# Kernel optimization log

Measured on AMD Instinct MI355X. Metric: run time of the kernel, lower is better.

## Reference

```python
import jax, jax.numpy as jnp
import numpy as np

N_MIN = 16
N_TABLES = 16
PER_LEVEL_SCALE = 1.3195079565048218
MAX_TABLE = 2 ** 19
H1, H2, H3 = 1, 2654435761, 805459861
OFFS = np.array([[0,0,0],[0,0,1],[0,1,0],[0,1,1],[1,0,0],[1,0,1],[1,1,0],[1,1,1]], dtype=np.int32)

def _levels():
    N_l, sizes, max_direct = [], [], 0
    for i in range(N_TABLES):
        res = int(np.ceil(N_MIN * np.exp(i * np.log(PER_LEVEL_SCALE)) - 1.0)) + 1
        ts = res ** 3
        ts = ts if ts % 8 == 0 else ((ts + 7) // 8) * 8
        ts = min(MAX_TABLE, ts)
        if ts == res ** 3:
            max_direct = i
        N_l.append(res); sizes.append(ts)
    return N_l, sizes, max_direct

N_L, SIZES, MAX_DIRECT = _levels()

def hash_encode(pos, grids):
    # pos: [N,3] in [0,1); grids: [16, MAX_TABLE, 2] (levels padded to MAX_TABLE)
    feats = []
    for l in range(N_TABLES):
        uvz = pos * jnp.float32(N_L[l])
        iuv_f = jnp.floor(uvz)
        f = uvz - iuv_f                                   # fractional part [N,3]
        corners = iuv_f.astype(jnp.int32)[:, None, :] + OFFS[None]  # [N,8,3]
        if l <= MAX_DIRECT:
            R = N_L[l]
            idx = (corners[..., 2] * (R * R) + corners[..., 1] * R + corners[..., 0]) % SIZES[l]
        else:
            cu = corners.astype(jnp.uint32)
            h = (cu[..., 0] * jnp.uint32(H1)) ^ (cu[..., 1] * jnp.uint32(H2)) ^ (cu[..., 2] * jnp.uint32(H3))
            idx = (h % jnp.uint32(SIZES[l])).astype(jnp.int32)
        c = grids[l][idx]                                 # gather -> [N,8,2]
        fx, fy, fz = f[:, 0:1], f[:, 1:2], f[:, 2:3]
        c00 = c[:, 0] * (1 - fx) + c[:, 4] * fx
        c01 = c[:, 1] * (1 - fx) + c[:, 5] * fx
        c10 = c[:, 2] * (1 - fx) + c[:, 6] * fx
        c11 = c[:, 3] * (1 - fx) + c[:, 7] * fx
        c0 = c00 * (1 - fy) + c10 * fy
        c1 = c01 * (1 - fy) + c11 * fy
        feats.append(c0 * (1 - fz) + c1 * fy)  # NOTE: c1*fy (not fz) replicates source exactly
    return jnp.concatenate(feats, axis=-1)  # [N, 32]

def setup_inputs():
    key = jax.random.key(0)
    ks = jax.random.split(key, 7)
    N = 1048576  # max_samples(512) * batch_size(2048)
    x = jax.random.uniform(ks[0], (N, 19), dtype=jnp.float32)  # pos(3) in [0,1) + dir feats(16)
    grids = (jax.random.uniform(ks[1], (N_TABLES, MAX_TABLE, 2), dtype=jnp.float32) * 2.0 - 1.0) * 1e-4
    h = 64
    w_sigma1 = jax.random.normal(ks[2], (32, h), dtype=jnp.float32) / np.sqrt(32).astype(np.float32)
    w_sigma2 = jax.random.normal(ks[3], (h, 16), dtype=jnp.float32) / np.sqrt(h).astype(np.float32)
    w_c1 = jax.random.normal(ks[4], (32, h), dtype=jnp.float32) / np.sqrt(32).astype(np.float32)
    w_c2 = jax.random.normal(ks[5], (h, h), dtype=jnp.float32) / np.sqrt(h).astype(np.float32)
    w_c3 = jax.random.normal(ks[6], (h, 3), dtype=jnp.float32) / np.sqrt(h).astype(np.float32)
    return {"x": x, "grids": grids, "w_sigma1": w_sigma1, "w_sigma2": w_sigma2,
            "w_c1": w_c1, "w_c2": w_c2, "w_c3": w_c3}

def reference(x, grids, w_sigma1, w_sigma2, w_c1, w_c2, w_c3):
    pos, direc = x[:, :3], x[:, 3:]
    enc = hash_encode(pos, grids)                       # [N,32]
    out = jax.nn.relu(enc @ w_sigma1) @ w_sigma2        # [N,16]
    sigma = out[:, 0]
    ci = jnp.concatenate([direc, out], axis=-1)         # [N,32]
    color = jax.nn.sigmoid(jax.nn.relu(jax.nn.relu(ci @ w_c1) @ w_c2) @ w_c3)  # [N,3]
    return jnp.concatenate([color, sigma[:, None]], axis=-1)  # [N,4]
```

## Files before the change

kernel.cpp:

```cpp
#include <hip/hip_runtime.h>
#include <math.h>


#define BLOCK 256
#define NTAB  (16*524288)
#define PITCH 88

constexpr int      kNL[16] = {16,22,28,37,49,65,85,112,148,195,257,338,446,589,777,1025};
constexpr unsigned kSZ[16] = {4096u,10648u,21952u,50656u,117656u,274632u,
                              524288u,524288u,524288u,524288u,524288u,
                              524288u,524288u,524288u,524288u,524288u};

typedef __attribute__((ext_vector_type(8))) short short8;
typedef __attribute__((ext_vector_type(4))) float float4v;

__device__ __forceinline__ short f2bf(float f) {
    unsigned u = __float_as_uint(f);
    unsigned r = u + 0x7fffu + ((u >> 16) & 1u);
    return (short)(r >> 16);
}
__device__ __forceinline__ float bf2f(short h) {
    return __uint_as_float(((unsigned)(unsigned short)h) << 16);
}
__device__ __forceinline__ unsigned pk2(float a, float b) {
    return ((unsigned)(unsigned short)f2bf(b) << 16) | (unsigned)(unsigned short)f2bf(a);
}
__device__ __forceinline__ float pe0(unsigned u) { return __uint_as_float(u << 16); }
__device__ __forceinline__ float pe1(unsigned u) { return __uint_as_float(u & 0xffff0000u); }

__global__ void pack_pos(const float* __restrict__ x, float4* __restrict__ pos4, int n)
{
    int i = blockIdx.x * BLOCK + threadIdx.x;
    if (i >= n) return;
    const float* xr = x + (size_t)i * 19;
    pos4[i] = make_float4(xr[0], xr[1], xr[2], 0.f);
}

__global__ void conv_tables(const float* __restrict__ grids, unsigned* __restrict__ tbu)
{
    int i = blockIdx.x * BLOCK + threadIdx.x;
    if (i >= NTAB) return;
    float2 v = ((const float2*)grids)[i];
    tbu[i] = pk2(v.x, v.y);
}

__global__ void pack_wfrag(const float* __restrict__ w1, const float* __restrict__ w2,
                           const float* __restrict__ wc1, const float* __restrict__ wc2,
                           const float* __restrict__ wc3, uint4* __restrict__ wf)
{
    int lane = threadIdx.x;
    if (lane >= 64) return;
    int cn = lane & 15, q = lane >> 4;

    auto pack8 = [](const float* src, int stride) -> uint4 {
        uint4 r;
        r.x = pk2(src[0*stride], src[1*stride]);
        r.y = pk2(src[2*stride], src[3*stride]);
        r.z = pk2(src[4*stride], src[5*stride]);
        r.w = pk2(src[6*stride], src[7*stride]);
        return r;
    };

    int f = 0;
    for (int nt = 0; nt < 4; ++nt)
        wf[(f++)*64 + lane] = pack8(w1 + (q*8)*64 + nt*16 + cn, 64);
    for (int c = 0; c < 2; ++c)
        wf[(f++)*64 + lane] = pack8(w2 + (c*32 + q*8)*16 + cn, 16);
    for (int nt = 0; nt < 4; ++nt)
        wf[(f++)*64 + lane] = pack8(wc1 + (q*8)*64 + nt*16 + cn, 64);
    for (int c = 0; c < 2; ++c)
        for (int nt = 0; nt < 4; ++nt)
            wf[(f++)*64 + lane] = pack8(wc2 + (c*32 + q*8)*64 + nt*16 + cn, 64);
    for (int c = 0; c < 2; ++c) {
        if (cn < 3) wf[(f++)*64 + lane] = pack8(wc3 + (c*32 + q*8)*3 + cn, 3);
        else { uint4 z; z.x = z.y = z.z = z.w = 0u; wf[(f++)*64 + lane] = z; }
    }
}

template<int L>
__device__ __forceinline__ void gather4(const float4* __restrict__ pos4,
                                        const unsigned* __restrict__ tball,
                                        unsigned* __restrict__ encu,
                                        int n, int p0, int cnt)
{
    constexpr int R = kNL[L];
    constexpr unsigned S = kSZ[L];
    constexpr unsigned H2c = 2654435761u, H3c = 805459861u;
    const unsigned* __restrict__ tbu = tball + (size_t)L * 524288u;

    unsigned vv[4][8];
    float fxa[4], fya[4], fza[4];
    #pragma unroll
    for (int q = 0; q < 4; ++q) {
        if (q >= cnt) continue;
        float4 p = pos4[p0+q];
        const float Rf = (float)R;
        float ux = p.x*Rf, uy = p.y*Rf, uz = p.z*Rf;
        float gx = floorf(ux), gy = floorf(uy), gz = floorf(uz);
        fxa[q] = ux-gx; fya[q] = uy-gy; fza[q] = uz-gz;
        int ix = (int)gx, iy = (int)gy, iz = (int)gz;

        if (L >= 6) {
            unsigned tc[4];
            #pragma unroll
            for (int c = 0; c < 4; ++c) {
                int yb = c >> 1, zb = c & 1;
                tc[c] = (unsigned)(iy+yb)*H2c ^ (unsigned)(iz+zb)*H3c;
            }
            if ((ix & 1) == 0) {
                #pragma unroll
                for (int c = 0; c < 4; ++c) {
                    unsigned idx0 = ((unsigned)ix ^ tc[c]) & (S-1u);
                    uint2 pr = *(const uint2*)(tbu + (idx0 & ~1u));
                    unsigned swp = idx0 & 1u;
                    vv[q][c]   = swp ? pr.y : pr.x;
                    vv[q][4+c] = swp ? pr.x : pr.y;
                }
            } else {
                #pragma unroll
                for (int c = 0; c < 4; ++c) {
                    unsigned idx0 = ((unsigned)ix     ^ tc[c]) & (S-1u);
                    unsigned idx1 = ((unsigned)(ix+1) ^ tc[c]) & (S-1u);
                    vv[q][c]   = tbu[idx0];
                    vv[q][4+c] = tbu[idx1];
                }
            }
        } else if (L >= 3) {
            #pragma unroll
            for (int j = 0; j < 8; ++j) {
                int ox = ix + ((j>>2)&1);
                int oy = iy + ((j>>1)&1);
                int oz = iz + (j&1);
                unsigned h = (unsigned)ox ^ (unsigned)oy*H2c ^ (unsigned)oz*H3c;
                vv[q][j] = tbu[h % S];
            }
        } else {
            #pragma unroll
            for (int j = 0; j < 8; ++j) {
                int ox = ix + ((j>>2)&1);
                int oy = iy + ((j>>1)&1);
                int oz = iz + (j&1);
                vv[q][j] = tbu[(unsigned)((oz*(R*R) + oy*R + ox) % (int)S)];
            }
        }
    }

    unsigned pkd[4];
    #pragma unroll
    for (int q = 0; q < 4; ++q) {
        if (q >= cnt) continue;
        const float fx = fxa[q], fy = fya[q], fz = fza[q];
        const float w0x = 1.f-fx, w0y = 1.f-fy, w0z = 1.f-fz;
        float e0, e1;
        {
            float c00 = pe0(vv[q][0])*w0x + pe0(vv[q][4])*fx;
            float c01 = pe0(vv[q][1])*w0x + pe0(vv[q][5])*fx;
            float c10 = pe0(vv[q][2])*w0x + pe0(vv[q][6])*fx;
            float c11 = pe0(vv[q][3])*w0x + pe0(vv[q][7])*fx;
            float c0 = c00*w0y + c10*fy;
            float c1 = c01*w0y + c11*fy;
            e0 = c0*w0z + c1*fy;
        }
        {
            float c00 = pe1(vv[q][0])*w0x + pe1(vv[q][4])*fx;
            float c01 = pe1(vv[q][1])*w0x + pe1(vv[q][5])*fx;
            float c10 = pe1(vv[q][2])*w0x + pe1(vv[q][6])*fx;
            float c11 = pe1(vv[q][3])*w0x + pe1(vv[q][7])*fx;
            float c0 = c00*w0y + c10*fy;
            float c1 = c01*w0y + c11*fy;
            e1 = c0*w0z + c1*fy;
        }
        pkd[q] = pk2(e0, e1);
    }

    unsigned* d = encu + (size_t)L*n + p0;
    if (cnt == 4) {
        uint4 o; o.x = pkd[0]; o.y = pkd[1]; o.z = pkd[2]; o.w = pkd[3];
        *(uint4*)d = o;
    } else {
        for (int q = 0; q < cnt; ++q) d[q] = pkd[q];
    }
}

__global__ __launch_bounds__(BLOCK)
void enc_all(const float4* __restrict__ pos4, const unsigned* __restrict__ tball,
             unsigned* __restrict__ encu, int n, int byA, int byB)
{
    const int bx = blockIdx.x;
    const int by = blockIdx.y;

    if (by < byA) {
        int p0 = (by*BLOCK + threadIdx.x) * 4;
        if (p0 >= n) return;
        int cnt = min(4, n - p0);
        switch (bx) {
            case 0: gather4< 6>(pos4,tball,encu,n,p0,cnt); break;
            case 1: gather4< 7>(pos4,tball,encu,n,p0,cnt); break;
            case 2: gather4< 8>(pos4,tball,encu,n,p0,cnt); break;
            case 3: gather4< 9>(pos4,tball,encu,n,p0,cnt); break;
            case 4: gather4<10>(pos4,tball,encu,n,p0,cnt); break;
            case 5: gather4<11>(pos4,tball,encu,n,p0,cnt); break;
            case 6: gather4<12>(pos4,tball,encu,n,p0,cnt); break;
            case 7: gather4<13>(pos4,tball,encu,n,p0,cnt); break;
        }
    } else if (by < byA + byB) {
        int q4 = (n + 3) / 4;
        int quarter = bx & 3;
        int jb = quarter * q4;
        int je = min(n, jb + q4);
        int p0 = jb + ((by-byA)*BLOCK + threadIdx.x) * 4;
        if (p0 >= je) return;
        int cnt = min(4, je - p0);
        if (bx < 4) gather4<14>(pos4,tball,encu,n,p0,cnt);
        else        gather4<15>(pos4,tball,encu,n,p0,cnt);
    } else {
        int cj = (by - byA - byB)*8 + bx;
        if (cj >= 6*byA) return;
        int level = cj % 6;
        int chunk = cj / 6;
        int p0 = (chunk*BLOCK + threadIdx.x) * 4;
        if (p0 >= n) return;
        int cnt = min(4, n - p0);
        switch (level) {
            case 0: gather4<0>(pos4,tball,encu,n,p0,cnt); break;
            case 1: gather4<1>(pos4,tball,encu,n,p0,cnt); break;
            case 2: gather4<2>(pos4,tball,encu,n,p0,cnt); break;
            case 3: gather4<3>(pos4,tball,encu,n,p0,cnt); break;
            case 4: gather4<4>(pos4,tball,encu,n,p0,cnt); break;
            case 5: gather4<5>(pos4,tball,encu,n,p0,cnt); break;
        }
    }
}

__device__ __forceinline__ short8 ldfrag(const uint4* __restrict__ wf, int f, int lane) {
    union { uint4 u; short8 s; } cv;
    cv.u = wf[f*64 + lane];
    return cv.s;
}

__global__ __launch_bounds__(BLOCK)
void mlp_mfma(const float* __restrict__ x,
              const unsigned* __restrict__ encu,
              const uint4* __restrict__ wf,
              float* __restrict__ out, int n)
{
    __shared__ unsigned short s_scr[4][2][16*PITCH];
    __shared__ float s_sig[4][16];
    __shared__ float s_col[4][16][4];

    const int t = threadIdx.x;
    const int lane = t & 63;
    const int wave = t >> 6;
    const int m = lane & 15;
    const int q = lane >> 4;
    const int cn = m;
    const int blk = blockIdx.x * 64;
    const int pt  = blk + wave*16 + m;
    const int ptc = pt < n ? pt : n - 1;

    const float4v zero = {0.f, 0.f, 0.f, 0.f};

    union { unsigned u[4]; short8 s; } a1;
    #pragma unroll
    for (int i = 0; i < 4; ++i)
        a1.u[i] = encu[(size_t)(q*4 + i)*n + ptc];

    short8 bw1[4], bw2[2], bwc1[4];
    #pragma unroll
    for (int nt = 0; nt < 4; ++nt) bw1[nt] = ldfrag(wf, nt, lane);
    #pragma unroll
    for (int c = 0; c < 2; ++c)    bw2[c]  = ldfrag(wf, 4 + c, lane);
    #pragma unroll
    for (int nt = 0; nt < 4; ++nt) bwc1[nt] = ldfrag(wf, 6 + nt, lane);

    float4v h[4];
    #pragma unroll
    for (int nt = 0; nt < 4; ++nt) {
        h[nt] = __builtin_amdgcn_mfma_f32_16x16x32_bf16(a1.s, bw1[nt], zero, 0, 0, 0);
        #pragma unroll
        for (int r = 0; r < 4; ++r) h[nt][r] = fmaxf(h[nt][r], 0.f);
    }

    unsigned short* sA = &s_scr[wave][0][0];
    unsigned short* sB = &s_scr[wave][1][0];
    #pragma unroll
    for (int nt = 0; nt < 4; ++nt)
        #pragma unroll
        for (int r = 0; r < 4; ++r)
            sA[(q*4+r)*PITCH + nt*16 + cn] = (unsigned short)f2bf(h[nt][r]);
    short8 ah[2];
    #pragma unroll
    for (int c = 0; c < 2; ++c)
        ah[c] = *(const short8*)&sA[m*PITCH + c*32 + q*8];

    float4v o = __builtin_amdgcn_mfma_f32_16x16x32_bf16(ah[0], bw2[0], zero, 0, 0, 0);
    o = __builtin_amdgcn_mfma_f32_16x16x32_bf16(ah[1], bw2[1], o, 0, 0, 0);
    if (cn == 0) {
        #pragma unroll
        for (int r = 0; r < 4; ++r) s_sig[wave][q*4+r] = o[r];
    }

    #pragma unroll
    for (int r = 0; r < 4; ++r)
        sB[(q*4+r)*PITCH + cn] = (unsigned short)f2bf(o[r]);
    short8 ov = *(const short8*)&sB[m*PITCH + (q >= 2 ? (q-2)*8 : 0)];

    union { unsigned u[4]; short8 s; } ci_hi, ci_lo;
    if (q < 2) {
        #pragma unroll
        for (int i = 0; i < 4; ++i) {
            float d0 = x[(size_t)ptc*19 + 3 + q*8 + 2*i];
            float d1 = x[(size_t)ptc*19 + 3 + q*8 + 2*i + 1];
            short h0 = f2bf(d0), h1 = f2bf(d1);
            ci_hi.u[i] = ((unsigned)(unsigned short)h1 << 16) | (unsigned)(unsigned short)h0;
            short l0 = f2bf(d0 - bf2f(h0)), l1 = f2bf(d1 - bf2f(h1));
            ci_lo.u[i] = ((unsigned)(unsigned short)l1 << 16) | (unsigned)(unsigned short)l0;
        }
    } else {
        ci_hi.s = ov;
        #pragma unroll
        for (int i = 0; i < 4; ++i) ci_lo.u[i] = 0u;
    }

    float4v hc[4];
    #pragma unroll
    for (int nt = 0; nt < 4; ++nt) {
        hc[nt] = __builtin_amdgcn_mfma_f32_16x16x32_bf16(ci_hi.s, bwc1[nt], zero, 0, 0, 0);
        hc[nt] = __builtin_amdgcn_mfma_f32_16x16x32_bf16(ci_lo.s, bwc1[nt], hc[nt], 0, 0, 0);
        #pragma unroll
        for (int r = 0; r < 4; ++r) hc[nt][r] = fmaxf(hc[nt][r], 0.f);
    }

    short8 bwc2[2][4], bwc3[2];
    #pragma unroll
    for (int c = 0; c < 2; ++c)
        #pragma unroll
        for (int nt = 0; nt < 4; ++nt)
            bwc2[c][nt] = ldfrag(wf, 10 + c*4 + nt, lane);
    #pragma unroll
    for (int c = 0; c < 2; ++c) bwc3[c] = ldfrag(wf, 18 + c, lane);

    #pragma unroll
    for (int nt = 0; nt < 4; ++nt)
        #pragma unroll
        for (int r = 0; r < 4; ++r) {
            float v = hc[nt][r];
            short hi = f2bf(v);
            sA[(q*4+r)*PITCH + nt*16 + cn] = (unsigned short)hi;
            sB[(q*4+r)*PITCH + nt*16 + cn] = (unsigned short)f2bf(v - bf2f(hi));
        }
    short8 ghi[2], glo[2];
    #pragma unroll
    for (int c = 0; c < 2; ++c) {
        ghi[c] = *(const short8*)&sA[m*PITCH + c*32 + q*8];
        glo[c] = *(const short8*)&sB[m*PITCH + c*32 + q*8];
    }

    float4v g[4];
    #pragma unroll
    for (int nt = 0; nt < 4; ++nt) {
        float4v acc = __builtin_amdgcn_mfma_f32_16x16x32_bf16(ghi[0], bwc2[0][nt], zero, 0, 0, 0);
        acc = __builtin_amdgcn_mfma_f32_16x16x32_bf16(glo[0], bwc2[0][nt], acc, 0, 0, 0);
        acc = __builtin_amdgcn_mfma_f32_16x16x32_bf16(ghi[1], bwc2[1][nt], acc, 0, 0, 0);
        acc = __builtin_amdgcn_mfma_f32_16x16x32_bf16(glo[1], bwc2[1][nt], acc, 0, 0, 0);
        #pragma unroll
        for (int r = 0; r < 4; ++r) acc[r] = fmaxf(acc[r], 0.f);
        g[nt] = acc;
    }

    #pragma unroll
    for (int nt = 0; nt < 4; ++nt)
        #pragma unroll
        for (int r = 0; r < 4; ++r) {
            float v = g[nt][r];
            short hi = f2bf(v);
            sA[(q*4+r)*PITCH + nt*16 + cn] = (unsigned short)hi;
            sB[(q*4+r)*PITCH + nt*16 + cn] = (unsigned short)f2bf(v - bf2f(hi));
        }
    short8 uhi[2], ulo[2];
    #pragma unroll
    for (int c = 0; c < 2; ++c) {
        uhi[c] = *(const short8*)&sA[m*PITCH + c*32 + q*8];
        ulo[c] = *(const short8*)&sB[m*PITCH + c*32 + q*8];
    }

    float4v col = __builtin_amdgcn_mfma_f32_16x16x32_bf16(uhi[0], bwc3[0], zero, 0, 0, 0);
    col = __builtin_amdgcn_mfma_f32_16x16x32_bf16(ulo[0], bwc3[0], col, 0, 0, 0);
    col = __builtin_amdgcn_mfma_f32_16x16x32_bf16(uhi[1], bwc3[1], col, 0, 0, 0);
    col = __builtin_amdgcn_mfma_f32_16x16x32_bf16(ulo[1], bwc3[1], col, 0, 0, 0);
    #pragma unroll
    for (int r = 0; r < 4; ++r)
        col[r] = 1.f / (1.f + __expf(-col[r]));

    if (cn < 3) {
        #pragma unroll
        for (int r = 0; r < 4; ++r) s_col[wave][q*4+r][cn] = col[r];
    }

    __builtin_amdgcn_s_waitcnt(0);
    int pfi = lane >> 2, c4 = lane & 3;
    int pout = blk + wave*16 + pfi;
    if (pout < n) {
        float v = (c4 == 3) ? s_sig[wave][pfi] : s_col[wave][pfi][c4];
        out[(size_t)pout*4 + c4] = v;
    }
}

extern "C" void kernel_launch(void* const* d_in, const int* in_sizes, int n_in,
                              void* d_out, int out_size, void* d_ws, size_t ws_size,
                              hipStream_t stream) {
    const float* x     = (const float*)d_in[0];
    const float* grids = (const float*)d_in[1];
    const float* w1    = (const float*)d_in[2];
    const float* w2    = (const float*)d_in[3];
    const float* wc1   = (const float*)d_in[4];
    const float* wc2   = (const float*)d_in[5];
    const float* wc3   = (const float*)d_in[6];
    float* out = (float*)d_out;

    int n = in_sizes[0] / 19;
    size_t encB = (size_t)16 * n * sizeof(unsigned);
    size_t posB = (size_t)n * sizeof(float4);
    size_t tabB = (size_t)NTAB * sizeof(unsigned);

    char* p = (char*)d_ws;
    unsigned* encu = (unsigned*)p;
    float4*   pos4 = (float4*)(p + encB);
    unsigned* tbu  = (unsigned*)(p + encB + posB);
    uint4*    wf   = (uint4*)(p + encB + posB + tabB);

    pack_pos<<<(n + BLOCK - 1) / BLOCK, BLOCK, 0, stream>>>(x, pos4, n);
    conv_tables<<<(NTAB + BLOCK - 1) / BLOCK, BLOCK, 0, stream>>>(grids, tbu);
    pack_wfrag<<<1, 64, 0, stream>>>(w1, w2, wc1, wc2, wc3, wf);

    int byA = (n + BLOCK*4 - 1) / (BLOCK*4);
    int q4  = (n + 3) / 4;
    int byB = (q4 + BLOCK*4 - 1) / (BLOCK*4);
    int jobsC = 6 * byA;
    int byC = (jobsC + 7) / 8;
    dim3 ge(8, byA + byB + byC);
    enc_all<<<ge, BLOCK, 0, stream>>>(pos4, tbu, encu, n, byA, byB);

    mlp_mfma<<<(n + 63) / 64, BLOCK, 0, stream>>>(x, encu, wf, out, n);
}
```

Before: 587.6 us.

## Fuse low-level encoding into MLP kernel and pair hashed-level corner loads

Levels 0-2 of the hash encoding are now computed inside the MLP kernel by 48 lanes per wave and passed through shared memory, so they are no longer written to and re-read from the global encoding buffer. The encoder's extra job list shrinks to levels 3-5. Direction features are staged into shared memory with coalesced loads instead of strided per-lane reads. For hashed levels 3-5, corner pairs with even ix are fetched with a single 64-bit load when the x-neighbour lands in the adjacent slot. The cost is extra gather latency and register pressure in the MLP kernel.

```diff
diff --git a/kernel.cpp b/kernel.cpp
--- a/kernel.cpp
+++ b/kernel.cpp
@@ -27,6 +27,31 @@
 }
 __device__ __forceinline__ float pe0(unsigned u) { return __uint_as_float(u << 16); }
 __device__ __forceinline__ float pe1(unsigned u) { return __uint_as_float(u & 0xffff0000u); }
+
+__device__ __forceinline__ unsigned trilerp_pack(const unsigned* vv, float fx, float fy, float fz)
+{
+    const float w0x = 1.f-fx, w0y = 1.f-fy, w0z = 1.f-fz;
+    float e0, e1;
+    {
+        float c00 = pe0(vv[0])*w0x + pe0(vv[4])*fx;
+        float c01 = pe0(vv[1])*w0x + pe0(vv[5])*fx;
+        float c10 = pe0(vv[2])*w0x + pe0(vv[6])*fx;
+        float c11 = pe0(vv[3])*w0x + pe0(vv[7])*fx;
+        float c0 = c00*w0y + c10*fy;
+        float c1 = c01*w0y + c11*fy;
+        e0 = c0*w0z + c1*fy;
+    }
+    {
+        float c00 = pe1(vv[0])*w0x + pe1(vv[4])*fx;
+        float c01 = pe1(vv[1])*w0x + pe1(vv[5])*fx;
+        float c10 = pe1(vv[2])*w0x + pe1(vv[6])*fx;
+        float c11 = pe1(vv[3])*w0x + pe1(vv[7])*fx;
+        float c0 = c00*w0y + c10*fy;
+        float c1 = c01*w0y + c11*fy;
+        e1 = c0*w0z + c1*fy;
+    }
+    return pk2(e0, e1);
+}
 
 __global__ void pack_pos(const float* __restrict__ x, float4* __restrict__ pos4, int n)
 {
@@ -126,13 +151,30 @@
                 }
             }
         } else if (L >= 3) {
+            unsigned tc[4];
             #pragma unroll
-            for (int j = 0; j < 8; ++j) {
-                int ox = ix + ((j>>2)&1);
-                int oy = iy + ((j>>1)&1);
-                int oz = iz + (j&1);
-                unsigned h = (unsigned)ox ^ (unsigned)oy*H2c ^ (unsigned)oz*H3c;
-                vv[q][j] = tbu[h % S];
+            for (int c = 0; c < 4; ++c) {
+                int yb = c >> 1, zb = c & 1;
+                tc[c] = (unsigned)(iy+yb)*H2c ^ (unsigned)(iz+zb)*H3c;
+            }
+            if ((ix & 1) == 0) {
+                #pragma unroll
+                for (int c = 0; c < 4; ++c) {
+                    unsigned h0 = (unsigned)ix ^ tc[c];
+                    unsigned base = (h0 & ~1u) % S;
+                    uint2 pr = *(const uint2*)(tbu + base);
+                    unsigned swp = h0 & 1u;
+                    vv[q][c]   = swp ? pr.y : pr.x;
+                    vv[q][4+c] = swp ? pr.x : pr.y;
+                }
+            } else {
+                #pragma unroll
+                for (int c = 0; c < 4; ++c) {
+                    unsigned h0 = ((unsigned)ix)     ^ tc[c];
+                    unsigned h1 = ((unsigned)(ix+1)) ^ tc[c];
+                    vv[q][c]   = tbu[h0 % S];
+                    vv[q][4+c] = tbu[h1 % S];
+                }
             }
         } else {
             #pragma unroll
@@ -149,28 +191,7 @@
     #pragma unroll
     for (int q = 0; q < 4; ++q) {
         if (q >= cnt) continue;
-        const float fx = fxa[q], fy = fya[q], fz = fza[q];
-        const float w0x = 1.f-fx, w0y = 1.f-fy, w0z = 1.f-fz;
-        float e0, e1;
-        {
-            float c00 = pe0(vv[q][0])*w0x + pe0(vv[q][4])*fx;
-            float c01 = pe0(vv[q][1])*w0x + pe0(vv[q][5])*fx;
-            float c10 = pe0(vv[q][2])*w0x + pe0(vv[q][6])*fx;
-            float c11 = pe0(vv[q][3])*w0x + pe0(vv[q][7])*fx;
-            float c0 = c00*w0y + c10*fy;
-            float c1 = c01*w0y + c11*fy;
-            e0 = c0*w0z + c1*fy;
-        }
-        {
-            float c00 = pe1(vv[q][0])*w0x + pe1(vv[q][4])*fx;
-            float c01 = pe1(vv[q][1])*w0x + pe1(vv[q][5])*fx;
-            float c10 = pe1(vv[q][2])*w0x + pe1(vv[q][6])*fx;
-            float c11 = pe1(vv[q][3])*w0x + pe1(vv[q][7])*fx;
-            float c0 = c00*w0y + c10*fy;
-            float c1 = c01*w0y + c11*fy;
-            e1 = c0*w0z + c1*fy;
-        }
-        pkd[q] = pk2(e0, e1);
+        pkd[q] = trilerp_pack(vv[q], fxa[q], fya[q], fza[q]);
     }
 
     unsigned* d = encu + (size_t)L*n + p0;
@@ -215,21 +236,40 @@
         else        gather4<15>(pos4,tball,encu,n,p0,cnt);
     } else {
         int cj = (by - byA - byB)*8 + bx;
-        if (cj >= 6*byA) return;
-        int level = cj % 6;
-        int chunk = cj / 6;
+        if (cj >= 3*byA) return;
+        int level = cj % 3;
+        int chunk = cj / 3;
         int p0 = (chunk*BLOCK + threadIdx.x) * 4;
         if (p0 >= n) return;
         int cnt = min(4, n - p0);
         switch (level) {
-            case 0: gather4<0>(pos4,tball,encu,n,p0,cnt); break;
-            case 1: gather4<1>(pos4,tball,encu,n,p0,cnt); break;
-            case 2: gather4<2>(pos4,tball,encu,n,p0,cnt); break;
-            case 3: gather4<3>(pos4,tball,encu,n,p0,cnt); break;
-            case 4: gather4<4>(pos4,tball,encu,n,p0,cnt); break;
-            case 5: gather4<5>(pos4,tball,encu,n,p0,cnt); break;
-        }
-    }
+            case 0: gather4<3>(pos4,tball,encu,n,p0,cnt); break;
+            case 1: gather4<4>(pos4,tball,encu,n,p0,cnt); break;
+            case 2: gather4<5>(pos4,tball,encu,n,p0,cnt); break;
+        }
+    }
+}
+
+template<int LV>
+__device__ __forceinline__ unsigned enc_low_t(float4 p, const unsigned* __restrict__ tball)
+{
+    constexpr int R = kNL[LV];
+    constexpr unsigned S = kSZ[LV];
+    const unsigned* __restrict__ tb = tball + (size_t)LV * 524288u;
+    const float Rf = (float)R;
+    float ux = p.x*Rf, uy = p.y*Rf, uz = p.z*Rf;
+    float gx = floorf(ux), gy = floorf(uy), gz = floorf(uz);
+    float fx = ux-gx, fy = uy-gy, fz = uz-gz;
+    int ix = (int)gx, iy = (int)gy, iz = (int)gz;
+    unsigned vv[8];
+    #pragma unroll
+    for (int j = 0; j < 8; ++j) {
+        int ox = ix + ((j>>2)&1);
+        int oy = iy + ((j>>1)&1);
+        int oz = iz + (j&1);
+        vv[j] = tb[(unsigned)((oz*(R*R) + oy*R + ox) % (int)S)];
+    }
+    return trilerp_pack(vv, fx, fy, fz);
 }
 
 __device__ __forceinline__ short8 ldfrag(const uint4* __restrict__ wf, int f, int lane) {
@@ -240,6 +280,8 @@
 
 __global__ __launch_bounds__(BLOCK)
 void mlp_mfma(const float* __restrict__ x,
+              const float4* __restrict__ pos4,
+              const unsigned* __restrict__ tbu,
               const unsigned* __restrict__ encu,
               const uint4* __restrict__ wf,
               float* __restrict__ out, int n)
@@ -247,6 +289,8 @@
     __shared__ unsigned short s_scr[4][2][16*PITCH];
     __shared__ float s_sig[4][16];
     __shared__ float s_col[4][16][4];
+    __shared__ float s_dir[4][304];
+    __shared__ unsigned s_low[4][3][16];
 
     const int t = threadIdx.x;
     const int lane = t & 63;
@@ -257,13 +301,44 @@
     const int blk = blockIdx.x * 64;
     const int pt  = blk + wave*16 + m;
     const int ptc = pt < n ? pt : n - 1;
+    const int p0w = blk + wave*16;
 
     const float4v zero = {0.f, 0.f, 0.f, 0.f};
 
+    {
+        int npts = n - p0w; if (npts > 16) npts = 16; if (npts < 0) npts = 0;
+        int nfl = npts * 19;
+        const float* xs = x + (size_t)p0w * 19;
+        float* sd = s_dir[wave];
+        #pragma unroll
+        for (int it = 0; it < 5; ++it) {
+            int idx = it*64 + lane;
+            if (idx < nfl) sd[idx] = xs[idx];
+        }
+    }
+
+    if (lane < 48) {
+        int lv = lane >> 4, pm = lane & 15;
+        int pp = p0w + pm; if (pp >= n) pp = n - 1;
+        float4 p = pos4[pp];
+        unsigned r;
+        if (lv == 0)      r = enc_low_t<0>(p, tbu);
+        else if (lv == 1) r = enc_low_t<1>(p, tbu);
+        else              r = enc_low_t<2>(p, tbu);
+        s_low[wave][lv][pm] = r;
+    }
+
     union { unsigned u[4]; short8 s; } a1;
-    #pragma unroll
-    for (int i = 0; i < 4; ++i)
-        a1.u[i] = encu[(size_t)(q*4 + i)*n + ptc];
+    if (q == 0) {
+        a1.u[0] = s_low[wave][0][m];
+        a1.u[1] = s_low[wave][1][m];
+        a1.u[2] = s_low[wave][2][m];
+        a1.u[3] = encu[(size_t)3*n + ptc];
+    } else {
+        #pragma unroll
+        for (int i = 0; i < 4; ++i)
+            a1.u[i] = encu[(size_t)(q*4 + i)*n + ptc];
+    }
 
     short8 bw1[4], bw2[2], bwc1[4];
     #pragma unroll
@@ -307,10 +382,12 @@
 
     union { unsigned u[4]; short8 s; } ci_hi, ci_lo;
     if (q < 2) {
+        const float* sd = s_dir[wave];
+        int rm = ptc - p0w; if (rm < 0) rm = 0;
         #pragma unroll
         for (int i = 0; i < 4; ++i) {
-            float d0 = x[(size_t)ptc*19 + 3 + q*8 + 2*i];
-            float d1 = x[(size_t)ptc*19 + 3 + q*8 + 2*i + 1];
+            float d0 = sd[rm*19 + 3 + q*8 + 2*i];
+            float d1 = sd[rm*19 + 3 + q*8 + 2*i + 1];
             short h0 = f2bf(d0), h1 = f2bf(d1);
             ci_hi.u[i] = ((unsigned)(unsigned short)h1 << 16) | (unsigned)(unsigned short)h0;
             short l0 = f2bf(d0 - bf2f(h0)), l1 = f2bf(d1 - bf2f(h1));
@@ -436,10 +513,10 @@
     int byA = (n + BLOCK*4 - 1) / (BLOCK*4);
     int q4  = (n + 3) / 4;
     int byB = (q4 + BLOCK*4 - 1) / (BLOCK*4);
-    int jobsC = 6 * byA;
+    int jobsC = 3 * byA;
     int byC = (jobsC + 7) / 8;
     dim3 ge(8, byA + byB + byC);
     enc_all<<<ge, BLOCK, 0, stream>>>(pos4, tbu, encu, n, byA, byB);
 
-    mlp_mfma<<<(n + 63) / 64, BLOCK, 0, stream>>>(x, encu, wf, out, n);
-}
+    mlp_mfma<<<(n + 63) / 64, BLOCK, 0, stream>>>(x, pos4, tbu, encu, wf, out, n);
+}
```

Result: faster. 563.5 us (-4.1%).
